# Kernel tuning notes

Hardware: AMD Instinct MI355X
Metric: run time of the kernel (lower is better)

Reference implementation:

```python
import jax, jax.numpy as jnp
import numpy as np

BN_EPS = 1e-5

def tanhshrink(x):
    return x - jnp.tanh(x)

def setup_inputs() -> dict:
    key = jax.random.key(0)
    ks = jax.random.split(key, 10)
    B, C, H, W = 32, 128, 32, 32
    RIN, RH, OC = 256, 512, 128
    s = lambda k, shape, fan: jax.random.normal(k, shape, dtype=jnp.float32) * (1.0 / np.sqrt(fan))
    return {
        "x": jax.random.normal(ks[0], (B, C, H, W), dtype=jnp.float32),
        "gamma": jnp.ones((C,), jnp.float32),
        "beta": jnp.zeros((C,), jnp.float32),
        "w_in": s(ks[1], (RIN, C), C),
        "b_in": jnp.zeros((RIN,), jnp.float32),
        "w_ih": s(ks[2], (RH, RIN), RIN),
        "b_ih": jnp.zeros((RH,), jnp.float32),
        "w_hh": s(ks[3], (RH, RH), RH),
        "b_hh": jnp.zeros((RH,), jnp.float32),
        "w_out": s(ks[4], (OC, RH), RH),
        "b_out": jnp.zeros((OC,), jnp.float32),
    }

def reference(x, gamma, beta, w_in, b_in, w_ih, b_ih, w_hh, b_hh, w_out, b_out):
    B, C, H, W = x.shape
    RH = w_hh.shape[0]
    # BatchNorm2d (training mode: batch statistics, biased variance)
    mean = jnp.mean(x, axis=(0, 2, 3), keepdims=True)
    var = jnp.var(x, axis=(0, 2, 3), keepdims=True)
    xn = (x - mean) * jax.lax.rsqrt(var + BN_EPS)
    xn = xn * gamma[None, :, None, None] + beta[None, :, None, None]
    # (B, L, C) sequence of flattened spatial locations
    seq = jnp.transpose(xn, (0, 2, 3, 1)).reshape(B, H * W, C)
    # Per-timestep Linear + Tanhshrink: has no recurrence, batch it over L
    inp = tanhshrink(jnp.einsum('blc,ic->bli', seq, w_in) + b_in)  # (B, L, RIN)
    # Precompute input contribution to RNNCell for all steps
    xgate = jnp.einsum('bli,hi->blh', inp, w_ih) + b_ih + b_hh  # (B, L, RH)
    xgate_t = jnp.transpose(xgate, (1, 0, 2))  # (L, B, RH)

    def step(h, xg):
        h_new = jnp.tanh(xg + h @ w_hh.T)
        return h_new, h_new

    h0 = jnp.zeros((B, RH), x.dtype)
    _, hs = jax.lax.scan(step, h0, xgate_t)  # (L, B, RH)
    outputs = jnp.transpose(hs, (1, 0, 2))  # (B, L, RH)
    out_seq = jnp.einsum('blh,oh->blo', outputs, w_out) + b_out  # (B, L, OC)
    out = jnp.transpose(out_seq.reshape(B, H, W, -1), (0, 3, 1, 2))
    return out
```

## Files before the change

kernel.cpp:

```cpp
#include <hip/hip_runtime.h>
#include <hip/hip_fp16.h>

typedef _Float16 f16;
typedef _Float16 f16x2 __attribute__((ext_vector_type(2)));
typedef _Float16 f16x8 __attribute__((ext_vector_type(8)));
typedef float    f32x4 __attribute__((ext_vector_type(4)));
typedef unsigned int u32;
typedef unsigned long long u64;

#define BN_EPS 1e-5f

static constexpr int BB  = 32;
static constexpr int CC  = 128;
static constexpr int HWN = 1024;
static constexpr int RIN = 256;
static constexpr int RH  = 512;
static constexpr int OCN = 128;

__global__ void bn_stats_kernel(const float* __restrict__ x,
                                const float* __restrict__ gamma,
                                const float* __restrict__ beta,
                                float* __restrict__ scale,
                                float* __restrict__ shift) {
    int c = blockIdx.x;
    int tid = threadIdx.x;
    float s = 0.f, s2 = 0.f;
    const float* xc = x + (size_t)c * HWN;
    for (int idx = tid; idx < BB * HWN; idx += 256) {
        int b = idx >> 10, hw = idx & 1023;
        float v = xc[(size_t)b * (CC * HWN) + hw];
        s += v; s2 += v * v;
    }
    for (int off = 32; off > 0; off >>= 1) {
        s  += __shfl_down(s, off, 64);
        s2 += __shfl_down(s2, off, 64);
    }
    __shared__ float ls[4], ls2[4];
    int wv = tid >> 6, ln = tid & 63;
    if (ln == 0) { ls[wv] = s; ls2[wv] = s2; }
    __syncthreads();
    if (tid == 0) {
        float ts  = ls[0] + ls[1] + ls[2] + ls[3];
        float ts2 = ls2[0] + ls2[1] + ls2[2] + ls2[3];
        const float inv_n = 1.0f / (BB * HWN);
        float mean = ts * inv_n;
        float var  = ts2 * inv_n - mean * mean;
        float rstd = rsqrtf(var + BN_EPS);
        float sc = gamma[c] * rstd;
        scale[c] = sc;
        shift[c] = beta[c] - mean * sc;
    }
}

__global__ void prep_x_kernel(const float* __restrict__ x,
                              const float* __restrict__ scale,
                              const float* __restrict__ shift,
                              f16* __restrict__ A1) {
    __shared__ float tile[32][33];
    int tx = threadIdx.x, ty = threadIdx.y;
    int hb = blockIdx.x, cb = blockIdx.y, b = blockIdx.z;
    #pragma unroll
    for (int k = 0; k < 4; k++) {
        int c  = cb * 32 + ty + 8 * k;
        int hw = hb * 32 + tx;
        tile[ty + 8 * k][tx] = x[(size_t)b * (CC * HWN) + (size_t)c * HWN + hw];
    }
    __syncthreads();
    #pragma unroll
    for (int k = 0; k < 4; k++) {
        int hw = hb * 32 + ty + 8 * k;
        int c  = cb * 32 + tx;
        float v = tile[tx][ty + 8 * k];
        A1[(size_t)(b * HWN + hw) * CC + c] = (f16)(v * scale[c] + shift[c]);
    }
}

__global__ void prep_w_kernel(const float* __restrict__ w_in,
                              const float* __restrict__ w_ih,
                              const float* __restrict__ w_out,
                              const float* __restrict__ w_hh,
                              const float* __restrict__ b_ih,
                              const float* __restrict__ b_hh,
                              f16* __restrict__ w_in_h,
                              f16* __restrict__ w_ih_h,
                              f16* __restrict__ w_out_h,
                              u32* __restrict__ wr,
                              float* __restrict__ bihh,
                              u64* __restrict__ comm) {
    int idx = blockIdx.x * 256 + threadIdx.x;
    if (idx < 32768) { w_in_h[idx] = (f16)w_in[idx]; return; }
    idx -= 32768;
    if (idx < 131072) { w_ih_h[idx] = (f16)w_ih[idx]; return; }
    idx -= 131072;
    if (idx < 65536) { w_out_h[idx] = (f16)w_out[idx]; return; }
    idx -= 65536;
    if (idx < 131072) {
        int s = idx >> 15, rem = idx & 32767;
        int t = rem >> 6, k = rem & 63;
        int r = k >> 4, n = k & 15;
        int jg = t & 31, sl = t >> 5;
        int j  = s * 128 + 4 * jg + r;
        int i2 = sl * 16 + n;
        f16 lo = (f16)w_hh[(size_t)j * 512 + 2 * i2];
        f16 hi = (f16)w_hh[(size_t)j * 512 + 2 * i2 + 1];
        wr[idx] = (u32)__builtin_bit_cast(unsigned short, lo) |
                  ((u32)__builtin_bit_cast(unsigned short, hi) << 16);
        return;
    }
    idx -= 131072;
    if (idx < 512) { bihh[idx] = b_ih[idx] + b_hh[idx]; return; }
    idx -= 512;
    if (idx < 32768) comm[idx] = 0ULL;
}

template <int MODE>
__global__ void gemm_kernel(const f16* __restrict__ A,
                            const f16* __restrict__ W,
                            const float* __restrict__ bias,
                            void* __restrict__ outp,
                            int N, int K) {
    int wave = threadIdx.x >> 6;
    int lane = threadIdx.x & 63;
    int q = lane >> 4, r = lane & 15;
    int bm = blockIdx.x * 256 + wave * 64;
    int bn = blockIdx.y * 64;

    f32x4 acc[4][4];
    #pragma unroll
    for (int i = 0; i < 4; i++)
        #pragma unroll
        for (int j = 0; j < 4; j++)
            acc[i][j] = (f32x4){0.f, 0.f, 0.f, 0.f};

    const f16* Ap = A + (size_t)(bm + r) * K + 8 * q;
    const f16* Wp = W + (size_t)(bn + r) * K + 8 * q;

    for (int k = 0; k < K; k += 32) {
        f16x8 av[4], bv[4];
        #pragma unroll
        for (int i = 0; i < 4; i++)
            av[i] = *(const f16x8*)(Ap + (size_t)(16 * i) * K + k);
        #pragma unroll
        for (int i = 0; i < 4; i++)
            bv[i] = *(const f16x8*)(Wp + (size_t)(16 * i) * K + k);
        #pragma unroll
        for (int mi = 0; mi < 4; mi++)
            #pragma unroll
            for (int ni = 0; ni < 4; ni++)
                acc[mi][ni] = __builtin_amdgcn_mfma_f32_16x16x32_f16(
                    av[mi], bv[ni], acc[mi][ni], 0, 0, 0);
    }

    #pragma unroll
    for (int mi = 0; mi < 4; mi++) {
        #pragma unroll
        for (int ni = 0; ni < 4; ni++) {
            int col = bn + 16 * ni + r;
            float bval = bias[col];
            #pragma unroll
            for (int i = 0; i < 4; i++) {
                int row = bm + 16 * mi + 4 * q + i;
                float val = acc[mi][ni][i] + bval;
                if (MODE == 0) {
                    val = val - tanhf(val);
                    ((f16*)outp)[(size_t)row * N + col] = (f16)val;
                } else if (MODE == 1) {
                    ((f16*)outp)[(size_t)row * N + col] = (f16)val;
                } else {
                    int b = row >> 10, hw = row & 1023;
                    ((float*)outp)[(size_t)b * (OCN * HWN) + (size_t)col * HWN + hw] = val;
                }
            }
        }
    }
}

__device__ __forceinline__ float dot2acc(u32 w, f16x2 h, float c) {
#if __has_builtin(__builtin_amdgcn_fdot2)
    return __builtin_amdgcn_fdot2(__builtin_bit_cast(f16x2, w), h, c, false);
#else
    f16x2 a = __builtin_bit_cast(f16x2, w);
    return c + (float)a[0] * (float)h[0] + (float)a[1] * (float)h[1];
#endif
}

#define ROW16(acc, WA, WB, WC, WD)                                  \
    acc = dot2acc(WA.x, H0,  acc); acc = dot2acc(WA.y, H1,  acc);   \
    acc = dot2acc(WA.z, H2,  acc); acc = dot2acc(WA.w, H3,  acc);   \
    acc = dot2acc(WB.x, H4,  acc); acc = dot2acc(WB.y, H5,  acc);   \
    acc = dot2acc(WB.z, H6,  acc); acc = dot2acc(WB.w, H7,  acc);   \
    acc = dot2acc(WC.x, H8,  acc); acc = dot2acc(WC.y, H9,  acc);   \
    acc = dot2acc(WC.z, H10, acc); acc = dot2acc(WC.w, H11, acc);   \
    acc = dot2acc(WD.x, H12, acc); acc = dot2acc(WD.y, H13, acc);   \
    acc = dot2acc(WD.z, H14, acc); acc = dot2acc(WD.w, H15, acc)

__global__ __launch_bounds__(512, 2) void rnn_kernel(const u32* WR,
                                                     f16* __restrict__ xh,
                                                     u64* slow, u64* fast) {
    const int wg = blockIdx.x;
    const int b  = wg & 31;
    const int s  = wg >> 5;
    const int t  = threadIdx.x;
    const int jg = t & 31;
    const int sl = t >> 5;

    __shared__ __align__(16) f16 hbuf[512];
    __shared__ float part[16][128];

    unsigned long long wpa =
        (unsigned long long)(WR + ((size_t)(s * 512 + t) << 6));
    asm volatile("" : "+v"(wpa));
    const uint4* wp = (const uint4*)wpa;
    uint4 W0 = wp[0],  W1 = wp[1],  W2 = wp[2],  W3 = wp[3];
    uint4 W4 = wp[4],  W5 = wp[5],  W6 = wp[6],  W7 = wp[7];
    uint4 W8 = wp[8],  W9 = wp[9],  W10 = wp[10], W11 = wp[11];
    uint4 W12 = wp[12], W13 = wp[13], W14 = wp[14], W15 = wp[15];

    if (t < 256) ((u32*)hbuf)[t] = 0u;
    __syncthreads();

    f16* xb = xh + (size_t)b * (HWN * RH) + s * 128;
    float xnext = 0.f;
    if (t < 128) xnext = (float)xb[t];

    u64* cbS = slow + (size_t)b * 256;
    u64* cbF = fast + (size_t)b * 256;
    const uint4* hq = (const uint4*)hbuf;

    for (int step = 0; step < HWN; step++) {
        float xcur = xnext;
        if (t < 128 && step + 1 < HWN)
            xnext = (float)xb[(size_t)(step + 1) * RH + t];

        uint4 q0 = hq[sl*4+0], q1 = hq[sl*4+1], q2 = hq[sl*4+2], q3 = hq[sl*4+3];
        f16x2 H0  = __builtin_bit_cast(f16x2, q0.x), H1  = __builtin_bit_cast(f16x2, q0.y);
        f16x2 H2  = __builtin_bit_cast(f16x2, q0.z), H3  = __builtin_bit_cast(f16x2, q0.w);
        f16x2 H4  = __builtin_bit_cast(f16x2, q1.x), H5  = __builtin_bit_cast(f16x2, q1.y);
        f16x2 H6  = __builtin_bit_cast(f16x2, q1.z), H7  = __builtin_bit_cast(f16x2, q1.w);
        f16x2 H8  = __builtin_bit_cast(f16x2, q2.x), H9  = __builtin_bit_cast(f16x2, q2.y);
        f16x2 H10 = __builtin_bit_cast(f16x2, q2.z), H11 = __builtin_bit_cast(f16x2, q2.w);
        f16x2 H12 = __builtin_bit_cast(f16x2, q3.x), H13 = __builtin_bit_cast(f16x2, q3.y);
        f16x2 H14 = __builtin_bit_cast(f16x2, q3.z), H15 = __builtin_bit_cast(f16x2, q3.w);
        float a0 = 0.f, a1 = 0.f, a2 = 0.f, a3 = 0.f;
        ROW16(a0, W0,  W1,  W2,  W3);
        ROW16(a1, W4,  W5,  W6,  W7);
        ROW16(a2, W8,  W9,  W10, W11);
        ROW16(a3, W12, W13, W14, W15);
        *(f32x4*)&part[sl][4 * jg] = (f32x4){a0, a1, a2, a3};
        __syncthreads();

        const u32 tag = (u32)(step + 1);
        const size_t pbase = (size_t)(tag & 1) * 8192;

        if (t >= 256 && t < 448) {
            int pi = (t - 256) >> 6;
            int widx = t & 63;
            int p = pi + (pi >= s ? 1 : 0);
            const u64* aF = &cbF[pbase + p * 64 + widx];
            u64* aS = &cbS[pbase + p * 64 + widx];
            u64 v;
            int guard = 0;
            for (;;) {
                asm volatile("global_load_dwordx2 %0, %1, off sc0\n\t"
                             "s_waitcnt vmcnt(0)"
                             : "=&v"(v) : "v"(aF) : "memory");
                if ((u32)(v >> 32) == tag) break;
                v = __hip_atomic_load(aS, __ATOMIC_RELAXED,
                                      __HIP_MEMORY_SCOPE_AGENT);
                if ((u32)(v >> 32) == tag) break;
                if (++guard > (1 << 17)) break;
            }
            ((u32*)hbuf)[p * 64 + widx] = (u32)v;
        }
        if (t < 128) {
            float y = xcur;
            #pragma unroll
            for (int k = 0; k < 16; k++) y += part[k][t];
            float h = tanhf(y);
            f16 hf = (f16)h;
            u32 hu = (u32)__builtin_bit_cast(unsigned short, hf);
            u32 other = (u32)__shfl_down((int)hu, 1, 64);
            if ((t & 1) == 0) {
                u64 v = ((u64)tag << 32) | (u64)(hu | (other << 16));
                __hip_atomic_store(&cbF[pbase + s * 64 + (t >> 1)], v,
                                   __ATOMIC_RELAXED, __HIP_MEMORY_SCOPE_WORKGROUP);
                __hip_atomic_store(&cbS[pbase + s * 64 + (t >> 1)], v,
                                   __ATOMIC_RELAXED, __HIP_MEMORY_SCOPE_AGENT);
            }
            hbuf[s * 128 + t] = hf;
            xb[(size_t)step * RH + t] = hf;
        }
        __syncthreads();
    }
}

extern "C" void kernel_launch(void* const* d_in, const int* in_sizes, int n_in,
                              void* d_out, int out_size, void* d_ws, size_t ws_size,
                              hipStream_t stream) {
    const float* x     = (const float*)d_in[0];
    const float* gamma = (const float*)d_in[1];
    const float* beta  = (const float*)d_in[2];
    const float* w_in  = (const float*)d_in[3];
    const float* b_in  = (const float*)d_in[4];
    const float* w_ih  = (const float*)d_in[5];
    const float* b_ih  = (const float*)d_in[6];
    const float* w_hh  = (const float*)d_in[7];
    const float* b_hh  = (const float*)d_in[8];
    const float* w_out = (const float*)d_in[9];
    const float* b_out = (const float*)d_in[10];

    char* ws = (char*)d_ws;
    float* scale   = (float*)(ws + 0);
    float* shift   = (float*)(ws + 512);
    float* bihh    = (float*)(ws + 1024);
    f16*   w_in_h  = (f16*)(ws + 4096);
    f16*   w_ih_h  = (f16*)(ws + 69632);
    f16*   w_out_h = (f16*)(ws + 331776);
    u32*   wr      = (u32*)(ws + 462848);
    u64*   cslow   = (u64*)(ws + 987136);
    u64*   cfast   = (u64*)(ws + 1118208);
    f16*   xh      = (f16*)(ws + 1310720);
    f16*   A1      = (f16*)(ws + 34865152);
    f16*   inp     = (f16*)(ws + 43253760);

    bn_stats_kernel<<<128, 256, 0, stream>>>(x, gamma, beta, scale, shift);
    prep_w_kernel<<<1538, 256, 0, stream>>>(w_in, w_ih, w_out, w_hh, b_ih, b_hh,
                                            w_in_h, w_ih_h, w_out_h, wr, bihh, cslow);
    prep_x_kernel<<<dim3(32, 4, 32), dim3(32, 8), 0, stream>>>(x, scale, shift, A1);
    gemm_kernel<0><<<dim3(128, 4), 256, 0, stream>>>(A1, w_in_h, b_in, (void*)inp, RIN, CC);
    gemm_kernel<1><<<dim3(128, 8), 256, 0, stream>>>(inp, w_ih_h, bihh, (void*)xh, RH, RIN);
    rnn_kernel<<<128, 512, 0, stream>>>(wr, xh, cslow, cfast);
    gemm_kernel<2><<<dim3(128, 2), 256, 0, stream>>>(xh, w_out_h, b_out, d_out, OCN, RH);
}
```

Measured before the change: 1.618 ms.

## Assign RNN tasks by XCD so batch groups share a die

The RNN kernel now launches 256 workgroups. Each one reads its hardware XCC ID and takes a rank on that XCD through global atomic counters, so the four slice workgroups of a batch element tend to land on the same XCD. Workgroups that were not placed wait for every workgroup to register, then fill the slots left open on under-populated XCDs, and the surplus exits early. Primary (co-located) groups poll the fast buffer and check the agent-scope buffer only now and then, while fallback groups poll the agent-scope buffer directly. A large LDS padding array caps residency per CU. The goal is to cut cross-die latency on the per-step h exchange, at the cost of a rendezvous spin that depends on every workgroup being resident at once.

```diff
diff --git a/kernel.cpp b/kernel.cpp
--- a/kernel.cpp
+++ b/kernel.cpp
@@ -86,7 +86,8 @@
                               f16* __restrict__ w_out_h,
                               u32* __restrict__ wr,
                               float* __restrict__ bihh,
-                              u64* __restrict__ comm) {
+                              u64* __restrict__ comm,
+                              u32* __restrict__ rz) {
     int idx = blockIdx.x * 256 + threadIdx.x;
     if (idx < 32768) { w_in_h[idx] = (f16)w_in[idx]; return; }
     idx -= 32768;
@@ -110,7 +111,9 @@
     idx -= 131072;
     if (idx < 512) { bihh[idx] = b_ih[idx] + b_hh[idx]; return; }
     idx -= 512;
-    if (idx < 32768) comm[idx] = 0ULL;
+    if (idx < 32768) { comm[idx] = 0ULL; return; }
+    idx -= 32768;
+    if (idx < 16) rz[idx] = 0u;
 }
 
 template <int MODE>
@@ -196,16 +199,60 @@
 
 __global__ __launch_bounds__(512, 2) void rnn_kernel(const u32* WR,
                                                      f16* __restrict__ xh,
-                                                     u64* slow, u64* fast) {
-    const int wg = blockIdx.x;
-    const int b  = wg & 31;
-    const int s  = wg >> 5;
-    const int t  = threadIdx.x;
+                                                     u64* slow, u64* fast,
+                                                     u32* rz) {
+    const int t = threadIdx.x;
+
+    __shared__ __align__(16) f16 hbuf[512];
+    __shared__ float part[16][128];
+    __shared__ u32 task_sh;
+    __shared__ u32 lds_pad[18432];
+
+    if (t == 0) {
+        u32 xcd;
+        asm volatile("s_getreg_b32 %0, hwreg(HW_REG_XCC_ID)" : "=s"(xcd));
+        xcd &= 7u;
+        u32 rank = __hip_atomic_fetch_add(&rz[1 + xcd], 1u,
+                                          __ATOMIC_RELAXED, __HIP_MEMORY_SCOPE_AGENT);
+        __hip_atomic_fetch_add(&rz[0], 1u,
+                               __ATOMIC_RELEASE, __HIP_MEMORY_SCOPE_AGENT);
+        u32 tk;
+        if (rank < 16u) {
+            tk = 0x8000u | (xcd * 16u + rank);
+        } else {
+            u32 orank = __hip_atomic_fetch_add(&rz[9], 1u,
+                                               __ATOMIC_RELAXED, __HIP_MEMORY_SCOPE_AGENT);
+            u32 g = 0;
+            while (__hip_atomic_load(&rz[0], __ATOMIC_ACQUIRE,
+                                     __HIP_MEMORY_SCOPE_AGENT) < 256u &&
+                   ++g < (1u << 27)) {}
+            tk = 0xFFFFFFFFu;
+            u32 acc = 0;
+            for (int x = 0; x < 8; x++) {
+                u32 c = __hip_atomic_load(&rz[1 + x], __ATOMIC_RELAXED,
+                                          __HIP_MEMORY_SCOPE_AGENT);
+                if (c > 16u) c = 16u;
+                u32 d = 16u - c;
+                if (orank < acc + d) {
+                    u32 r2 = c + (orank - acc);
+                    tk = (u32)x * 16u + r2;
+                    break;
+                }
+                acc += d;
+            }
+        }
+        task_sh = tk;
+    }
+    if (t < 256) ((u32*)hbuf)[t] = 0u;
+    __syncthreads();
+    const u32 task = task_sh;
+    if (task == 0xFFFFFFFFu) return;
+    if (task == 0x7FFFFFFFu) lds_pad[t] = t;
+    const int primary = (task >> 15) & 1;
+    const int b = (task & 127) >> 2;
+    const int s = task & 3;
     const int jg = t & 31;
     const int sl = t >> 5;
-
-    __shared__ __align__(16) f16 hbuf[512];
-    __shared__ float part[16][128];
 
     unsigned long long wpa =
         (unsigned long long)(WR + ((size_t)(s * 512 + t) << 6));
@@ -215,9 +262,6 @@
     uint4 W4 = wp[4],  W5 = wp[5],  W6 = wp[6],  W7 = wp[7];
     uint4 W8 = wp[8],  W9 = wp[9],  W10 = wp[10], W11 = wp[11];
     uint4 W12 = wp[12], W13 = wp[13], W14 = wp[14], W15 = wp[15];
-
-    if (t < 256) ((u32*)hbuf)[t] = 0u;
-    __syncthreads();
 
     f16* xb = xh + (size_t)b * (HWN * RH) + s * 128;
     float xnext = 0.f;
@@ -259,16 +303,28 @@
             const u64* aF = &cbF[pbase + p * 64 + widx];
             u64* aS = &cbS[pbase + p * 64 + widx];
             u64 v;
-            int guard = 0;
-            for (;;) {
-                asm volatile("global_load_dwordx2 %0, %1, off sc0\n\t"
-                             "s_waitcnt vmcnt(0)"
-                             : "=&v"(v) : "v"(aF) : "memory");
-                if ((u32)(v >> 32) == tag) break;
-                v = __hip_atomic_load(aS, __ATOMIC_RELAXED,
-                                      __HIP_MEMORY_SCOPE_AGENT);
-                if ((u32)(v >> 32) == tag) break;
-                if (++guard > (1 << 17)) break;
+            u32 g = 0;
+            if (primary) {
+                for (;;) {
+                    asm volatile("global_load_dwordx2 %0, %1, off sc0\n\t"
+                                 "s_waitcnt vmcnt(0)"
+                                 : "=&v"(v) : "v"(aF) : "memory");
+                    if ((u32)(v >> 32) == tag) break;
+                    ++g;
+                    if ((g & 7u) == 7u) {
+                        v = __hip_atomic_load(aS, __ATOMIC_RELAXED,
+                                              __HIP_MEMORY_SCOPE_AGENT);
+                        if ((u32)(v >> 32) == tag) break;
+                    }
+                    if (g > (1u << 17)) break;
+                }
+            } else {
+                for (;;) {
+                    v = __hip_atomic_load(aS, __ATOMIC_RELAXED,
+                                          __HIP_MEMORY_SCOPE_AGENT);
+                    if ((u32)(v >> 32) == tag) break;
+                    if (++g > (1u << 17)) break;
+                }
             }
             ((u32*)hbuf)[p * 64 + widx] = (u32)v;
         }
@@ -319,16 +375,18 @@
     u32*   wr      = (u32*)(ws + 462848);
     u64*   cslow   = (u64*)(ws + 987136);
     u64*   cfast   = (u64*)(ws + 1118208);
+    u32*   rz      = (u32*)(ws + 1249280);
     f16*   xh      = (f16*)(ws + 1310720);
     f16*   A1      = (f16*)(ws + 34865152);
     f16*   inp     = (f16*)(ws + 43253760);
 
     bn_stats_kernel<<<128, 256, 0, stream>>>(x, gamma, beta, scale, shift);
-    prep_w_kernel<<<1538, 256, 0, stream>>>(w_in, w_ih, w_out, w_hh, b_ih, b_hh,
-                                            w_in_h, w_ih_h, w_out_h, wr, bihh, cslow);
+    prep_w_kernel<<<1539, 256, 0, stream>>>(w_in, w_ih, w_out, w_hh, b_ih, b_hh,
+                                            w_in_h, w_ih_h, w_out_h, wr, bihh,
+                                            cslow, rz);
     prep_x_kernel<<<dim3(32, 4, 32), dim3(32, 8), 0, stream>>>(x, scale, shift, A1);
     gemm_kernel<0><<<dim3(128, 4), 256, 0, stream>>>(A1, w_in_h, b_in, (void*)inp, RIN, CC);
     gemm_kernel<1><<<dim3(128, 8), 256, 0, stream>>>(inp, w_ih_h, bihh, (void*)xh, RH, RIN);
-    rnn_kernel<<<128, 512, 0, stream>>>(wr, xh, cslow, cfast);
+    rnn_kernel<<<256, 512, 0, stream>>>(wr, xh, cslow, cfast, rz);
     gemm_kernel<2><<<dim3(128, 2), 256, 0, stream>>>(xh, w_out_h, b_out, d_out, OCN, RH);
 }
```

Result: slower. 2.216 ms (+36.9%).
